# Kernel optimization log

Measured on AMD Instinct MI355X. Metric: run time of the kernel, lower is better.

## Reference

```python
import jax, jax.numpy as jnp
import numpy as np

H = 12          # n_heads
TYPE = 0        # center node type (query path)
EDGES = (0, 4, 5)  # useful_edge for type==0
NEG = -1e10
LN_EPS = 1e-5


def _type_emb(x, W, b, t):
    # Linear(E -> 2E), view [N,2,E], scatter-mask select type t (uniform type -> index)
    h = x @ W.T + b
    N = x.shape[0]
    E = W.shape[0] // 2
    return h.reshape(N, 2, E)[:, t, :]


def _layernorm(x, g, b):
    mu = jnp.mean(x, axis=-1, keepdims=True)
    var = jnp.mean((x - mu) ** 2, axis=-1, keepdims=True)
    return g * (x - mu) / jnp.sqrt(var + LN_EPS) + b


def setup_inputs() -> dict:
    B, L, E, R = 64, 64, 768, 8
    dk = E // H
    key = jax.random.key(0)
    ks = jax.random.split(key, 16)
    s = 0.02
    inp = {
        'center_ids': jax.random.randint(ks[0], (B, L), 0, 5000),
        'centers': jax.random.normal(ks[1], (B * L, E), jnp.float32),
        'all_embs': jax.random.normal(ks[2], (2 * B * L, E), jnp.float32),
        'pre_mask': (jax.random.uniform(ks[3], (B, L, L)) < 0.3).astype(jnp.float32),
        'back_mask': (jax.random.uniform(ks[4], (B, L, L)) < 0.3).astype(jnp.float32),
        'click_mask': (jax.random.uniform(ks[5], (B, L, L)) < 0.3).astype(jnp.float32),
        'blank': jnp.zeros((B, L, L), jnp.float32),
        'Wq': jax.random.normal(ks[6], (2 * E, E), jnp.float32) * s,
        'bq': jnp.zeros((2 * E,), jnp.float32),
        'Wk': jax.random.normal(ks[7], (2 * E, E), jnp.float32) * s,
        'bk': jnp.zeros((2 * E,), jnp.float32),
        'Wv': jax.random.normal(ks[8], (2 * E, E), jnp.float32) * s,
        'bv': jnp.zeros((2 * E,), jnp.float32),
        'Wa': jax.random.normal(ks[9], (2 * E, E), jnp.float32) * s,
        'ba': jnp.zeros((2 * E,), jnp.float32),
        'relation_pri': jnp.ones((R, H), jnp.float32),
        'relation_att': jax.random.normal(ks[10], (R, H, dk, dk), jnp.float32) / np.sqrt(dk),
        'relation_msg': jax.random.normal(ks[11], (R, H, dk, dk), jnp.float32) / np.sqrt(dk),
        'skip': jnp.ones((3,), jnp.float32),
        'ln_gamma': jnp.ones((E,), jnp.float32),
        'ln_beta': jnp.zeros((E,), jnp.float32),
    }
    return inp


def reference(center_ids, centers, all_embs, pre_mask, back_mask, click_mask, blank,
              Wq, bq, Wk, bk, Wv, bv, Wa, ba,
              relation_pri, relation_att, relation_msg, skip, ln_gamma, ln_beta):
    B, L = center_ids.shape
    E = centers.shape[-1]
    dk = E // H
    BL = B * L
    sqrt_dk = np.sqrt(dk).astype(np.float32)

    # type-masked QKV projections (q: all type 0; k,v: first BL type 0, second BL type 1)
    q = _type_emb(centers, Wq, bq, TYPE)                       # [BL, E]
    hk = (all_embs @ Wk.T + bk).reshape(2 * BL, 2, E)
    k = jnp.concatenate([hk[:BL, 0], hk[BL:, 1]], axis=0)      # [2BL, E]
    hv = (all_embs @ Wv.T + bv).reshape(2 * BL, 2, E)
    v = jnp.concatenate([hv[:BL, 0], hv[BL:, 1]], axis=0)      # [2BL, E]

    q4 = q.reshape(B, L, H, dk).transpose(2, 0, 1, 3)                          # [H,B,L,dk]
    k4 = k.reshape(2, B, L, H, dk).transpose(3, 1, 0, 2, 4).reshape(H, B, 2 * L, dk)
    v4 = v.reshape(2, B, L, H, dk).transpose(3, 1, 0, 2, 4).reshape(H, B, 2 * L, dk)

    eidx = jnp.array(EDGES)
    ra = relation_att[eidx]   # [3,H,dk,dk]
    rm = relation_msg[eidx]   # [3,H,dk,dk]
    pri = relation_pri[eidx]  # [3,H]

    kproj = jnp.einsum('hbtd,ehdf->ehbtf', k4, ra)                                  # [3,H,B,2L,dk]
    att = jnp.einsum('hbld,ehbtd->ehblt', q4, kproj) * pri[:, :, None, None, None] / sqrt_dk
    msg = jnp.einsum('hbtd,ehdf->ehbtf', v4, rm)                                    # [3,H,B,2L,dk]

    # flatten (kv_pos, edge) in the torch cat/view order: index = t*3 + e
    A = att.transpose(1, 2, 3, 4, 0).reshape(H, B, L, 2 * L * 3)
    msgf = msg.transpose(1, 2, 3, 0, 4).reshape(H, B, 2 * L * 3, dk)

    # per-edge masks for type==0: edge0 -> [blank|click], edge1 -> [back|blank], edge2 -> [pre|blank]
    m0 = jnp.concatenate([blank, click_mask], axis=-1)
    m1 = jnp.concatenate([back_mask, blank], axis=-1)
    m2 = jnp.concatenate([pre_mask, blank], axis=-1)
    mask = jnp.stack([m0, m1, m2], axis=-1).reshape(B, L, 2 * L * 3) > 0            # [B,L,TE]

    # share masks among identical center ids (equality is transitive => one matmul = closure)
    same = center_ids[:, :, None] == center_ids[:, None, :]                         # [B,L,L]
    repeat = jnp.triu(same, 1).sum(1) > 0                                           # [B,L]
    add = jnp.einsum('bil,blj->bij', same.astype(jnp.float32), mask.astype(jnp.float32)) > 0
    mask = (mask | add) & (~repeat[:, :, None])

    scores = jnp.where(mask[None], A, NEG)
    p = jax.nn.softmax(scores, axis=-1) * mask[None].astype(A.dtype)
    neigh = jnp.einsum('hblt,hbtd->hbld', p, msgf).transpose(1, 2, 0, 3).reshape(BL, E)
    neigh = jax.nn.gelu(neigh, approximate=False)

    retype = _type_emb(neigh, Wa, ba, TYPE)
    alpha = jax.nn.sigmoid(skip[TYPE])
    res = retype * alpha + centers * (1.0 - alpha)
    out = _layernorm(res, ln_gamma, ln_beta)
    return out.reshape(B, L, E)
```

## Files before the change

kernel.cpp:

```cpp
#include <hip/hip_runtime.h>
#include <cmath>

#define NEGV -1e10f

typedef __bf16 bf16_t;
typedef bf16_t bf16x8 __attribute__((ext_vector_type(8)));
typedef bf16_t bf16x4 __attribute__((ext_vector_type(4)));
typedef float f32x4 __attribute__((ext_vector_type(4)));

typedef const __attribute__((address_space(1))) void* gas1p;
typedef __attribute__((address_space(3))) void* las3p;

#define MFMA __builtin_amdgcn_mfma_f32_16x16x32_bf16

__global__ __launch_bounds__(256)
void prep_kernel(const int* __restrict__ ids, const float* __restrict__ pre,
                 const float* __restrict__ back, const float* __restrict__ click,
                 unsigned long long* __restrict__ msk64,
                 const float* __restrict__ rmsg, const float* __restrict__ ratt,
                 const float* __restrict__ pri, bf16_t* __restrict__ rmT, bf16_t* __restrict__ raB,
                 const float* __restrict__ s0, bf16_t* __restrict__ d0,
                 const float* __restrict__ s1, bf16_t* __restrict__ d1,
                 const float* __restrict__ s2, bf16_t* __restrict__ d2,
                 const float* __restrict__ s3, bf16_t* __restrict__ d3,
                 const float* __restrict__ s4, bf16_t* __restrict__ d4,
                 const float* __restrict__ s5, bf16_t* __restrict__ d5) {
  const int bid = blockIdx.x, tid = threadIdx.x;
  __shared__ float pm[64][68], bmm[64][68], cm[64][68];
  __shared__ unsigned long long sbits[64];
  __shared__ unsigned long long colbits[384];
  __shared__ int sid[64];
  __shared__ unsigned char srep[64];
  if (bid < 64) {
    const int b = bid;
    for (int r = 0; r < 4; ++r) {
      int idx = r*256 + tid; int row = idx >> 4; int c4 = (idx & 15) * 4;
      *(float4*)&pm[row][c4]  = *(const float4*)(pre   + (size_t)b*4096 + row*64 + c4);
      *(float4*)&bmm[row][c4] = *(const float4*)(back  + (size_t)b*4096 + row*64 + c4);
      *(float4*)&cm[row][c4]  = *(const float4*)(click + (size_t)b*4096 + row*64 + c4);
    }
    if (tid < 64) sid[tid] = ids[b*64 + tid];
    __syncthreads();
    if (tid < 64) {
      int myid = sid[tid];
      unsigned long long bits = 0ull; int rep = 0;
      for (int l = 0; l < 64; ++l) {
        bool eq = (sid[l] == myid);
        bits |= ((unsigned long long)eq) << l;
        rep |= (eq && (l < tid)) ? 1 : 0;
      }
      sbits[tid] = bits; srep[tid] = (unsigned char)rep;
    }
    for (int j = tid; j < 384; j += 256) {
      int e = j >> 7, t = j & 127;
      unsigned long long cb = 0ull;
      if (e == 0) {
        if (t >= 64) { int tt = t - 64; for (int l = 0; l < 64; ++l) cb |= ((unsigned long long)(cm[l][tt] > 0.0f)) << l; }
      } else if (e == 1) {
        if (t < 64) { for (int l = 0; l < 64; ++l) cb |= ((unsigned long long)(bmm[l][t] > 0.0f)) << l; }
      } else {
        if (t < 64) { for (int l = 0; l < 64; ++l) cb |= ((unsigned long long)(pm[l][t] > 0.0f)) << l; }
      }
      colbits[j] = cb;
    }
    __syncthreads();
    for (int idx = tid; idx < 384; idx += 256) {
      int l = idx / 6, w = idx - l*6;
      unsigned long long r = 0ull;
      if (!srep[l]) {
        unsigned long long sb = sbits[l];
        const int base = w*64;
        for (int jj = 0; jj < 64; ++jj)
          r |= (unsigned long long)((sb & colbits[base + jj]) != 0ull) << jj;
      }
      msk64[((size_t)(b*64) + l)*6 + w] = r;
    }
    return;
  }
  if (bid < 100) {
    const int eh = bid - 64;
    const int e = eh / 12, h = eh - e*12;
    const int re = (e==0) ? 0 : (e==1 ? 4 : 5);
    const float scale = pri[re*12 + h] * 0.125f;
    for (int i = 0; i < 16; ++i) {
      int idx = i*256 + tid;
      int d = idx >> 6, f = idx & 63;
      rmT[((size_t)(e*12 + h)*64 + d)*64 + f] =
          (bf16_t)rmsg[((size_t)(re*12 + h)*64 + f)*64 + d];
      raB[((size_t)(e*12 + h)*64 + d)*64 + f] =
          (bf16_t)(ratt[((size_t)(re*12 + h)*64 + d)*64 + f] * scale);
    }
    return;
  }
  const int N0=786432, N1=1572864, N2=147456, N3=294912, N4=294912, N5=147456;
  const int T = N0+N1+N2+N3+N4+N5;
  int i = (bid - 100) * 256 + tid;
  const int stride = (gridDim.x - 100) * 256;
  for (; i < T; i += stride) {
    const float* s; bf16_t* d; int j = i;
    if (j < N0) { s = s0; d = d0; }
    else { j -= N0; if (j < N1) { s = s1; d = d1; }
    else { j -= N1; if (j < N2) { s = s2; d = d2; }
    else { j -= N2; if (j < N3) { s = s3; d = d3; }
    else { j -= N3; if (j < N4) { s = s4; d = d4; }
    else { j -= N4; s = s5; d = d5; } } } } }
    float4 v = *(const float4*)(s + (size_t)j * 4);
    bf16x4 o = { (bf16_t)v.x, (bf16_t)v.y, (bf16_t)v.z, (bf16_t)v.w };
    *(bf16x4*)(d + (size_t)j * 4) = o;
  }
}

__global__ __launch_bounds__(256)
void proj_mfmaB(const bf16_t* __restrict__ X, const bf16_t* __restrict__ W,
                const float* __restrict__ bias, bf16_t* __restrict__ Y) {
  __shared__ bf16_t As[128 * 32];
  __shared__ bf16_t Bs[128 * 32];
  const int bn = blockIdx.x, bm = blockIdx.y;
  const int row0 = bm * 128, col0 = bn * 128;
  const int tid = threadIdx.x, wave = tid >> 6, lane = tid & 63;
  const int wr = wave >> 1, wc = wave & 1;
  f32x4 acc[4][4] = {};
  const int arow = wr * 64 + (lane & 15);
  const int bcol = wc * 64 + (lane & 15);
  const int koff = (lane >> 4) * 8;
  for (int k0 = 0; k0 < 768; k0 += 32) {
    __syncthreads();
    #pragma unroll
    for (int i = 0; i < 2; ++i) {
      int c = i * 256 + tid; int r = c >> 2; int c8 = (c & 3) * 8;
      __builtin_amdgcn_global_load_lds((gas1p)(X + (size_t)(row0 + r) * 768 + k0 + c8),
                                       (las3p)(As + c * 8), 16, 0, 0);
      __builtin_amdgcn_global_load_lds((gas1p)(W + (size_t)(col0 + r) * 768 + k0 + c8),
                                       (las3p)(Bs + c * 8), 16, 0, 0);
    }
    __syncthreads();
    bf16x8 af[4], bfr[4];
    #pragma unroll
    for (int m = 0; m < 4; ++m) af[m]  = *(const bf16x8*)(As + (arow + m * 16) * 32 + koff);
    #pragma unroll
    for (int n = 0; n < 4; ++n) bfr[n] = *(const bf16x8*)(Bs + (bcol + n * 16) * 32 + koff);
    #pragma unroll
    for (int m = 0; m < 4; ++m)
      #pragma unroll
      for (int n = 0; n < 4; ++n)
        acc[m][n] = MFMA(af[m], bfr[n], acc[m][n], 0, 0, 0);
  }
  const int ocol0 = col0 + wc * 64 + (lane & 15);
  const int orow0 = row0 + wr * 64 + (lane >> 4) * 4;
  #pragma unroll
  for (int n = 0; n < 4; ++n) {
    const int col = ocol0 + n * 16;
    const float bvl = bias[col];
    #pragma unroll
    for (int m = 0; m < 4; ++m)
      #pragma unroll
      for (int r = 0; r < 4; ++r)
        Y[(size_t)(orow0 + m * 16 + r) * 768 + col] = (bf16_t)(acc[m][n][r] + bvl);
  }
}

__global__ __launch_bounds__(256)
void proj_mfmaF(const bf16_t* __restrict__ X, const bf16_t* __restrict__ W,
                const float* __restrict__ bias, float* __restrict__ Y) {
  __shared__ bf16_t As[128 * 32];
  __shared__ bf16_t Bs[128 * 32];
  const int bn = blockIdx.x, bm = blockIdx.y;
  const int row0 = bm * 128, col0 = bn * 128;
  const int tid = threadIdx.x, wave = tid >> 6, lane = tid & 63;
  const int wr = wave >> 1, wc = wave & 1;
  f32x4 acc[4][4] = {};
  const int arow = wr * 64 + (lane & 15);
  const int bcol = wc * 64 + (lane & 15);
  const int koff = (lane >> 4) * 8;
  for (int k0 = 0; k0 < 768; k0 += 32) {
    __syncthreads();
    #pragma unroll
    for (int i = 0; i < 2; ++i) {
      int c = i * 256 + tid; int r = c >> 2; int c8 = (c & 3) * 8;
      __builtin_amdgcn_global_load_lds((gas1p)(X + (size_t)(row0 + r) * 768 + k0 + c8),
                                       (las3p)(As + c * 8), 16, 0, 0);
      __builtin_amdgcn_global_load_lds((gas1p)(W + (size_t)(col0 + r) * 768 + k0 + c8),
                                       (las3p)(Bs + c * 8), 16, 0, 0);
    }
    __syncthreads();
    bf16x8 af[4], bfr[4];
    #pragma unroll
    for (int m = 0; m < 4; ++m) af[m]  = *(const bf16x8*)(As + (arow + m * 16) * 32 + koff);
    #pragma unroll
    for (int n = 0; n < 4; ++n) bfr[n] = *(const bf16x8*)(Bs + (bcol + n * 16) * 32 + koff);
    #pragma unroll
    for (int m = 0; m < 4; ++m)
      #pragma unroll
      for (int n = 0; n < 4; ++n)
        acc[m][n] = MFMA(af[m], bfr[n], acc[m][n], 0, 0, 0);
  }
  const int ocol0 = col0 + wc * 64 + (lane & 15);
  const int orow0 = row0 + wr * 64 + (lane >> 4) * 4;
  #pragma unroll
  for (int n = 0; n < 4; ++n) {
    const int col = ocol0 + n * 16;
    const float bvl = bias[col];
    #pragma unroll
    for (int m = 0; m < 4; ++m)
      #pragma unroll
      for (int r = 0; r < 4; ++r)
        Y[(size_t)(orow0 + m * 16 + r) * 768 + col] = acc[m][n][r] + bvl;
  }
}

__global__ __launch_bounds__(256)
void kv_proj(const bf16_t* __restrict__ X, const bf16_t* __restrict__ Wk,
             const bf16_t* __restrict__ Wv, const float* __restrict__ bk,
             const float* __restrict__ bv, bf16_t* __restrict__ K, bf16_t* __restrict__ VT) {
  __shared__ bf16_t As[128 * 32];
  __shared__ bf16_t Bks[128 * 32];
  __shared__ bf16_t Bvs[128 * 32];
  __shared__ char tl[128 * 256];
  const int bn = blockIdx.x, bm = blockIdx.y;
  const int s = (bm >= 32) ? 1 : 0;
  const int row0 = bm * 128, col0 = bn * 128;
  const int tid = threadIdx.x, wave = tid >> 6, lane = tid & 63;
  const int wr = wave >> 1, wc = wave & 1;
  f32x4 acck[4][4] = {};
  f32x4 accv[4][4] = {};
  const int arow = wr * 64 + (lane & 15);
  const int bcol = wc * 64 + (lane & 15);
  const int koff = (lane >> 4) * 8;
  const bf16_t* Wkb = Wk + (size_t)s * 768 * 768;
  const bf16_t* Wvb = Wv + (size_t)s * 768 * 768;
  for (int k0 = 0; k0 < 768; k0 += 32) {
    __syncthreads();
    #pragma unroll
    for (int i = 0; i < 2; ++i) {
      int c = i * 256 + tid; int r = c >> 2; int c8 = (c & 3) * 8;
      __builtin_amdgcn_global_load_lds((gas1p)(X   + (size_t)(row0 + r) * 768 + k0 + c8),
                                       (las3p)(As  + c * 8), 16, 0, 0);
      __builtin_amdgcn_global_load_lds((gas1p)(Wkb + (size_t)(col0 + r) * 768 + k0 + c8),
                                       (las3p)(Bks + c * 8), 16, 0, 0);
      __builtin_amdgcn_global_load_lds((gas1p)(Wvb + (size_t)(col0 + r) * 768 + k0 + c8),
                                       (las3p)(Bvs + c * 8), 16, 0, 0);
    }
    __syncthreads();
    bf16x8 af[4], bk_[4], bv_[4];
    #pragma unroll
    for (int m = 0; m < 4; ++m) af[m]  = *(const bf16x8*)(As  + (arow + m * 16) * 32 + koff);
    #pragma unroll
    for (int n = 0; n < 4; ++n) { bk_[n] = *(const bf16x8*)(Bks + (bcol + n * 16) * 32 + koff);
                                  bv_[n] = *(const bf16x8*)(Bvs + (bcol + n * 16) * 32 + koff); }
    #pragma unroll
    for (int m = 0; m < 4; ++m)
      #pragma unroll
      for (int n = 0; n < 4; ++n) {
        acck[m][n] = MFMA(af[m], bk_[n], acck[m][n], 0, 0, 0);
        accv[m][n] = MFMA(af[m], bv_[n], accv[m][n], 0, 0, 0);
      }
  }
  const int ocol0 = col0 + wc * 64 + (lane & 15);
  const int orow0 = row0 + wr * 64 + (lane >> 4) * 4;
  #pragma unroll
  for (int n = 0; n < 4; ++n) {
    const int col = ocol0 + n * 16;
    const float bvl = bk[s * 768 + col];
    #pragma unroll
    for (int m = 0; m < 4; ++m)
      #pragma unroll
      for (int r = 0; r < 4; ++r)
        K[(size_t)(orow0 + m * 16 + r) * 768 + col] = (bf16_t)(acck[m][n][r] + bvl);
  }
  #pragma unroll
  for (int n = 0; n < 4; ++n) {
    const int cl = wc * 64 + n * 16 + (lane & 15);
    const float bvl = bv[s * 768 + col0 + cl];
    #pragma unroll
    for (int m = 0; m < 4; ++m)
      #pragma unroll
      for (int r = 0; r < 4; ++r) {
        const int rl = wr * 64 + m * 16 + (lane >> 4) * 4 + r;
        *(bf16_t*)(tl + ((cl * 256 + rl * 2) ^ ((cl & 7) << 4))) = (bf16_t)(accv[m][n][r] + bvl);
      }
  }
  __syncthreads();
  for (int i = 0; i < 8; ++i) {
    int idx = i * 256 + tid; int c = idx >> 4; int t0 = (idx & 15) * 8;
    bf16x8 v = *(const bf16x8*)(tl + ((c * 256 + t0 * 2) ^ ((c & 7) << 4)));
    *(bf16x8*)(VT + (size_t)(col0 + c) * 8192 + row0 + t0) = v;
  }
}

__global__ __launch_bounds__(256, 2)
void attn_fused2(const bf16_t* __restrict__ qraw, const bf16_t* __restrict__ kb,
                 const bf16_t* __restrict__ vT, const bf16_t* __restrict__ rmT,
                 const bf16_t* __restrict__ raB,
                 const unsigned long long* __restrict__ msk64,
                 bf16_t* __restrict__ neigh) {
  const int h = blockIdx.x, b = blockIdx.y;
  __shared__ char lds[81920];
  char* const QLS  = lds;
  char* const RALS = lds + 8192;
  char* const QELS = lds + 32768;
  char* const VLS  = lds;
  char* const PLS  = lds + 16384;
  char* const KLS  = lds + 32768;
  char* const RMLS = lds + 49152;
  char* const USS  = lds + 73728;
  const int tid = threadIdx.x, wave = tid >> 6, lane = tid & 63;
  const int band = wave * 16, colb = lane & 15;

  bf16x8 qreg[2], rareg[6], kreg[4], vreg[4], rmreg[6];
  #pragma unroll
  for (int i = 0; i < 2; ++i) { int idx = i*256 + tid; int l = idx >> 3, f0 = (idx & 7) * 8;
    qreg[i] = *(const bf16x8*)(qraw + (size_t)(b*64 + l)*768 + h*64 + f0); }
  #pragma unroll
  for (int i = 0; i < 6; ++i) { int idx = i*256 + tid; int e = idx >> 9, rem = idx & 511, d = rem >> 3, f0 = (rem & 7) * 8;
    rareg[i] = *(const bf16x8*)(raB + (size_t)((e*12 + h)*64 + d)*64 + f0); }
  #pragma unroll
  for (int i = 0; i < 4; ++i) { int idx = i*256 + tid; int t = idx >> 3, c8 = (idx & 7) * 8;
    int srow = (t >> 6)*4096 + b*64 + (t & 63);
    kreg[i] = *(const bf16x8*)(kb + (size_t)srow*768 + h*64 + c8); }
  #pragma unroll
  for (int i = 0; i < 4; ++i) { int idx = i*256 + tid; int f = idx >> 4, t0 = (idx & 15) * 8;
    vreg[i] = *(const bf16x8*)(vT + (size_t)(h*64 + f)*8192 + (t0 >> 6)*4096 + b*64 + (t0 & 63)); }
  #pragma unroll
  for (int i = 0; i < 6; ++i) { int idx = i*256 + tid; int e = idx >> 9, rem = idx & 511, d = rem >> 3, f0 = (rem & 7) * 8;
    rmreg[i] = *(const bf16x8*)(rmT + (size_t)((e*12 + h)*64 + d)*64 + f0); }

  #pragma unroll
  for (int i = 0; i < 2; ++i) { int idx = i*256 + tid; int l = idx >> 3, f0 = (idx & 7) * 8;
    *(bf16x8*)(QLS + ((l*128 + f0*2) ^ ((l & 7) << 4))) = qreg[i]; }
  #pragma unroll
  for (int i = 0; i < 6; ++i) { int idx = i*256 + tid; int e = idx >> 9, rem = idx & 511, d = rem >> 3, f0 = (rem & 7) * 8;
    *(bf16x8*)(RALS + e*8192 + ((d*128 + f0*2) ^ ((d & 7) << 4))) = rareg[i]; }
  __syncthreads();
  f32x4 accq[3][4] = {};
  #pragma unroll
  for (int ks = 0; ks < 2; ++ks) {
    const int kb2 = (ks*32 + (lane >> 4)*8) * 2;
    const int la = band + colb;
    bf16x8 a = *(const bf16x8*)(QLS + ((la*128 + kb2) ^ ((la & 7) << 4)));
    #pragma unroll
    for (int e = 0; e < 3; ++e)
      #pragma unroll
      for (int n = 0; n < 4; ++n) {
        int d = n*16 + colb;
        bf16x8 bf = *(const bf16x8*)(RALS + e*8192 + ((d*128 + kb2) ^ ((d & 7) << 4)));
        accq[e][n] = MFMA(a, bf, accq[e][n], 0, 0, 0);
      }
  }
  #pragma unroll
  for (int e = 0; e < 3; ++e)
    #pragma unroll
    for (int n = 0; n < 4; ++n)
      #pragma unroll
      for (int r = 0; r < 4; ++r) {
        int l = band + (lane >> 4)*4 + r, d = n*16 + colb;
        *(bf16_t*)(QELS + e*8192 + ((l*128 + d*2) ^ ((l & 7) << 4))) = (bf16_t)accq[e][n][r];
      }
  __syncthreads();
  bf16x8 af[3][2];
  #pragma unroll
  for (int e = 0; e < 3; ++e)
    #pragma unroll
    for (int ks = 0; ks < 2; ++ks) {
      int la = band + colb, kd2 = (ks*32 + (lane >> 4)*8) * 2;
      af[e][ks] = *(const bf16x8*)(QELS + e*8192 + ((la*128 + kd2) ^ ((la & 7) << 4)));
    }
  __syncthreads();
  #pragma unroll
  for (int i = 0; i < 4; ++i) { int idx = i*256 + tid; int t = idx >> 3, c8 = (idx & 7) * 8;
    *(bf16x8*)(KLS + ((t*128 + c8*2) ^ ((t & 7) << 4))) = kreg[i]; }
  #pragma unroll
  for (int i = 0; i < 4; ++i) { int idx = i*256 + tid; int f = idx >> 4, t0 = (idx & 15) * 8;
    *(bf16x8*)(VLS + ((f*256 + t0*2) ^ ((f & 7) << 4))) = vreg[i]; }
  #pragma unroll
  for (int i = 0; i < 6; ++i) { int idx = i*256 + tid; int e = idx >> 9, rem = idx & 511, d = rem >> 3, f0 = (rem & 7) * 8;
    *(bf16x8*)(RMLS + e*8192 + ((d*128 + f0*2) ^ ((d & 7) << 4))) = rmreg[i]; }
  __syncthreads();
  f32x4 acc[3][8] = {};
  #pragma unroll
  for (int ks = 0; ks < 2; ++ks) {
    bf16x8 bfr[8];
    #pragma unroll
    for (int n = 0; n < 8; ++n) {
      int t = n*16 + colb;
      bfr[n] = *(const bf16x8*)(KLS + ((t*128 + (ks*32 + (lane >> 4)*8)*2) ^ ((t & 7) << 4)));
    }
    #pragma unroll
    for (int e = 0; e < 3; ++e)
      #pragma unroll
      for (int n = 0; n < 8; ++n)
        acc[e][n] = MFMA(af[e][ks], bfr[n], acc[e][n], 0, 0, 0);
  }
  float mx[4], inv[4];
  #pragma unroll
  for (int r = 0; r < 4; ++r) {
    const int l = band + (lane >> 4)*4 + r;
    const unsigned long long* mr = msk64 + (size_t)(b*64 + l)*6;
    #pragma unroll
    for (int e = 0; e < 3; ++e) {
      unsigned long long w0 = mr[e*2], w1 = mr[e*2 + 1];
      #pragma unroll
      for (int n = 0; n < 8; ++n) {
        unsigned long long w = (n < 4) ? w0 : w1;
        int bitpos = (n*16 + colb) & 63;
        if (!((w >> bitpos) & 1ull)) acc[e][n][r] = NEGV;
      }
    }
  }
  #pragma unroll
  for (int r = 0; r < 4; ++r) {
    float m = NEGV;
    #pragma unroll
    for (int e = 0; e < 3; ++e)
      #pragma unroll
      for (int n = 0; n < 8; ++n) m = fmaxf(m, acc[e][n][r]);
    #pragma unroll
    for (int off = 1; off < 16; off <<= 1) m = fmaxf(m, __shfl_xor(m, off, 64));
    mx[r] = m;
  }
  #pragma unroll
  for (int r = 0; r < 4; ++r) {
    float s = 0.0f;
    #pragma unroll
    for (int e = 0; e < 3; ++e)
      #pragma unroll
      for (int n = 0; n < 8; ++n) {
        float v = __expf(acc[e][n][r] - mx[r]);
        acc[e][n][r] = v; s += v;
      }
    #pragma unroll
    for (int off = 1; off < 16; off <<= 1) s += __shfl_xor(s, off, 64);
    inv[r] = (mx[r] < -5e9f) ? 0.0f : 1.0f / s;
  }
  f32x4 accN[4] = {};
  #pragma unroll
  for (int e = 0; e < 3; ++e) {
    #pragma unroll
    for (int n = 0; n < 8; ++n)
      #pragma unroll
      for (int r = 0; r < 4; ++r) {
        int l = band + (lane >> 4)*4 + r;
        int t = n*16 + colb;
        *(bf16_t*)(PLS + ((l*256 + t*2) ^ ((l & 7) << 4))) = (bf16_t)(acc[e][n][r] * inv[r]);
      }
    __syncthreads();
    f32x4 accU[4] = {};
    #pragma unroll
    for (int ks = 0; ks < 4; ++ks) {
      const int kb2 = (ks*32 + (lane >> 4)*8) * 2;
      const int la = band + colb;
      bf16x8 a = *(const bf16x8*)(PLS + ((la*256 + kb2) ^ ((la & 7) << 4)));
      #pragma unroll
      for (int n = 0; n < 4; ++n) {
        int f = n*16 + colb;
        bf16x8 bv = *(const bf16x8*)(VLS + ((f*256 + kb2) ^ ((f & 7) << 4)));
        accU[n] = MFMA(a, bv, accU[n], 0, 0, 0);
      }
    }
    #pragma unroll
    for (int n = 0; n < 4; ++n)
      #pragma unroll
      for (int r = 0; r < 4; ++r) {
        int l = band + (lane >> 4)*4 + r;
        int f = n*16 + colb;
        *(bf16_t*)(USS + ((l*128 + f*2) ^ ((l & 7) << 4))) = (bf16_t)accU[n][r];
      }
    __syncthreads();
    #pragma unroll
    for (int ks = 0; ks < 2; ++ks) {
      const int kb2 = (ks*32 + (lane >> 4)*8) * 2;
      const int la = band + colb;
      bf16x8 a2 = *(const bf16x8*)(USS + ((la*128 + kb2) ^ ((la & 7) << 4)));
      #pragma unroll
      for (int n = 0; n < 4; ++n) {
        int d = n*16 + colb;
        bf16x8 brm = *(const bf16x8*)(RMLS + e*8192 + ((d*128 + kb2) ^ ((d & 7) << 4)));
        accN[n] = MFMA(a2, brm, accN[n], 0, 0, 0);
      }
    }
  }
  #pragma unroll
  for (int n = 0; n < 4; ++n)
    #pragma unroll
    for (int r = 0; r < 4; ++r) {
      int l = band + (lane >> 4)*4 + r;
      int d = n*16 + colb;
      float x = accN[n][r];
      float g = 0.5f * x * (1.0f + erff(x * 0.70710678118654752f));
      neigh[(size_t)(b*64 + l)*768 + h*64 + d] = (bf16_t)g;
    }
}

__global__ __launch_bounds__(256)
void ln_kernel(const float* __restrict__ rt, const float* __restrict__ centers,
               const float* __restrict__ skip, const float* __restrict__ gamma,
               const float* __restrict__ beta, float* __restrict__ out) {
  const int row  = blockIdx.x*4 + (threadIdx.x >> 6);
  const int lane = threadIdx.x & 63;
  const float alpha = 1.0f / (1.0f + expf(-skip[0]));
  const float* rp = rt + (size_t)row*768;
  const float* cp = centers + (size_t)row*768;
  float r[12];
  float sum = 0.0f;
  #pragma unroll
  for (int c = 0; c < 12; ++c) {
    int j = lane + 64*c;
    float x = alpha*rp[j] + (1.0f - alpha)*cp[j];
    r[c] = x; sum += x;
  }
  #pragma unroll
  for (int off = 1; off < 64; off <<= 1) sum += __shfl_xor(sum, off, 64);
  float mean = sum * (1.0f/768.0f);
  float vsum = 0.0f;
  #pragma unroll
  for (int c = 0; c < 12; ++c) { float d = r[c] - mean; vsum += d*d; }
  #pragma unroll
  for (int off = 1; off < 64; off <<= 1) vsum += __shfl_xor(vsum, off, 64);
  float inv = 1.0f / sqrtf(vsum * (1.0f/768.0f) + 1e-5f);
  #pragma unroll
  for (int c = 0; c < 12; ++c) {
    int j = lane + 64*c;
    out[(size_t)row*768 + j] = gamma[j]*(r[c] - mean)*inv + beta[j];
  }
}

extern "C" void kernel_launch(void* const* d_in, const int* in_sizes, int n_in,
                              void* d_out, int out_size, void* d_ws, size_t ws_size,
                              hipStream_t stream) {
  const int*   ids     = (const int*)  d_in[0];
  const float* centers = (const float*)d_in[1];
  const float* allemb  = (const float*)d_in[2];
  const float* pre     = (const float*)d_in[3];
  const float* back    = (const float*)d_in[4];
  const float* click   = (const float*)d_in[5];
  const float* Wq = (const float*)d_in[7];
  const float* bq = (const float*)d_in[8];
  const float* Wk = (const float*)d_in[9];
  const float* bk = (const float*)d_in[10];
  const float* Wv = (const float*)d_in[11];
  const float* bv = (const float*)d_in[12];
  const float* Wa = (const float*)d_in[13];
  const float* ba = (const float*)d_in[14];
  const float* pri  = (const float*)d_in[15];
  const float* ratt = (const float*)d_in[16];
  const float* rmsg = (const float*)d_in[17];
  const float* skip = (const float*)d_in[18];
  const float* gam  = (const float*)d_in[19];
  const float* bet  = (const float*)d_in[20];
  float* out = (float*)d_out;

  char* wp = (char*)d_ws;
  bf16_t* cen_bf = (bf16_t*)wp;  wp += 6291456;
  bf16_t* all_bf = (bf16_t*)wp;  wp += 12582912;
  bf16_t* Wq_bf  = (bf16_t*)wp;  wp += 1179648;
  bf16_t* Wk_bf  = (bf16_t*)wp;  wp += 2359296;
  bf16_t* Wv_bf  = (bf16_t*)wp;  wp += 2359296;
  bf16_t* Wa_bf  = (bf16_t*)wp;  wp += 1179648;
  bf16_t* rmT    = (bf16_t*)wp;  wp += 294912;
  bf16_t* raB    = (bf16_t*)wp;  wp += 294912;
  bf16_t* qraw   = (bf16_t*)wp;  wp += 6291456;
  bf16_t* kb     = (bf16_t*)wp;  wp += 12582912;
  bf16_t* vTb    = (bf16_t*)wp;  wp += 12582912;
  unsigned long long* msk64 = (unsigned long long*)wp; wp += 196608;
  bf16_t* neighb = (bf16_t*)wp;  wp += 6291456;
  float*  rt     = (float*)wp;   wp += 12582912;

  prep_kernel<<<dim3(2048), 256, 0, stream>>>(
      ids, pre, back, click, msk64, rmsg, ratt, pri, rmT, raB,
      centers, cen_bf, allemb, all_bf, Wq, Wq_bf, Wk, Wk_bf, Wv, Wv_bf, Wa, Wa_bf);

  proj_mfmaB<<<dim3(6, 32), 256, 0, stream>>>(cen_bf, Wq_bf, bq, qraw);
  kv_proj   <<<dim3(6, 64), 256, 0, stream>>>(all_bf, Wk_bf, Wv_bf, bk, bv, kb, vTb);

  attn_fused2<<<dim3(12, 64), 256, 0, stream>>>(qraw, kb, vTb, rmT, raB, msk64, neighb);

  proj_mfmaF<<<dim3(6, 32), 256, 0, stream>>>(neighb, Wa_bf, ba, rt);
  ln_kernel<<<dim3(1024), 256, 0, stream>>>(rt, centers, skip, gam, bet, out);
}
```

Measured before the change: 266.8 us.

## Merge Q and KV projections into one double-buffered launch

Replaces the separate Q projection and KV projection kernels with a single qkv_proj kernel whose grid covers both: the first 32 row-blocks do the Q GEMM and the rest do the fused K/V GEMM. The k-loop now double-buffers its LDS tiles, issuing the next tile's async global-to-LDS loads before computing on the current one, with one barrier per step instead of two. This removes one kernel launch and tail, lets Q and KV blocks share the GPU together, and overlaps load latency with MFMA work. The cost is more LDS per block (48KB), which may lower occupancy, plus a Q/KV branch that mixes light and heavy blocks in one grid.

```diff
diff --git a/kernel.cpp b/kernel.cpp
--- a/kernel.cpp
+++ b/kernel.cpp
@@ -111,51 +111,137 @@
 }
 
 __global__ __launch_bounds__(256)
-void proj_mfmaB(const bf16_t* __restrict__ X, const bf16_t* __restrict__ W,
-                const float* __restrict__ bias, bf16_t* __restrict__ Y) {
-  __shared__ bf16_t As[128 * 32];
-  __shared__ bf16_t Bs[128 * 32];
-  const int bn = blockIdx.x, bm = blockIdx.y;
+void qkv_proj(const bf16_t* __restrict__ cen, const bf16_t* __restrict__ allb,
+              const bf16_t* __restrict__ Wq, const bf16_t* __restrict__ Wk,
+              const bf16_t* __restrict__ Wv,
+              const float* __restrict__ bq, const float* __restrict__ bk,
+              const float* __restrict__ bv,
+              bf16_t* __restrict__ Q, bf16_t* __restrict__ K, bf16_t* __restrict__ VT) {
+  __shared__ char lds[49152];
+  const int bn = blockIdx.x, by = blockIdx.y;
+  const bool qmode = (by < 32);
+  const int bm = qmode ? by : (by - 32);
+  const int s = (!qmode && bm >= 32) ? 1 : 0;
   const int row0 = bm * 128, col0 = bn * 128;
+  const bf16_t* X  = qmode ? cen : allb;
+  const bf16_t* WA = qmode ? Wq : (Wk + (size_t)s * 768 * 768);
+  const bf16_t* WB = Wv + (size_t)s * 768 * 768;
   const int tid = threadIdx.x, wave = tid >> 6, lane = tid & 63;
   const int wr = wave >> 1, wc = wave & 1;
-  f32x4 acc[4][4] = {};
   const int arow = wr * 64 + (lane & 15);
   const int bcol = wc * 64 + (lane & 15);
   const int koff = (lane >> 4) * 8;
-  for (int k0 = 0; k0 < 768; k0 += 32) {
-    __syncthreads();
+  f32x4 acck[4][4] = {};
+  f32x4 accv[4][4] = {};
+
+  {
+    bf16_t* As  = (bf16_t*)(lds);
+    bf16_t* Bks = As + 4096;
+    bf16_t* Bvs = As + 8192;
     #pragma unroll
     for (int i = 0; i < 2; ++i) {
       int c = i * 256 + tid; int r = c >> 2; int c8 = (c & 3) * 8;
-      __builtin_amdgcn_global_load_lds((gas1p)(X + (size_t)(row0 + r) * 768 + k0 + c8),
+      __builtin_amdgcn_global_load_lds((gas1p)(X  + (size_t)(row0 + r) * 768 + c8),
                                        (las3p)(As + c * 8), 16, 0, 0);
-      __builtin_amdgcn_global_load_lds((gas1p)(W + (size_t)(col0 + r) * 768 + k0 + c8),
-                                       (las3p)(Bs + c * 8), 16, 0, 0);
-    }
-    __syncthreads();
-    bf16x8 af[4], bfr[4];
-    #pragma unroll
-    for (int m = 0; m < 4; ++m) af[m]  = *(const bf16x8*)(As + (arow + m * 16) * 32 + koff);
-    #pragma unroll
-    for (int n = 0; n < 4; ++n) bfr[n] = *(const bf16x8*)(Bs + (bcol + n * 16) * 32 + koff);
-    #pragma unroll
-    for (int m = 0; m < 4; ++m)
-      #pragma unroll
-      for (int n = 0; n < 4; ++n)
-        acc[m][n] = MFMA(af[m], bfr[n], acc[m][n], 0, 0, 0);
-  }
+      __builtin_amdgcn_global_load_lds((gas1p)(WA + (size_t)(col0 + r) * 768 + c8),
+                                       (las3p)(Bks + c * 8), 16, 0, 0);
+      if (!qmode)
+        __builtin_amdgcn_global_load_lds((gas1p)(WB + (size_t)(col0 + r) * 768 + c8),
+                                         (las3p)(Bvs + c * 8), 16, 0, 0);
+    }
+  }
+  __syncthreads();
+
+  for (int k = 0; k < 24; ++k) {
+    if (k < 23) {
+      const int k0 = (k + 1) * 32;
+      bf16_t* As  = (bf16_t*)(lds + ((k + 1) & 1) * 24576);
+      bf16_t* Bks = As + 4096;
+      bf16_t* Bvs = As + 8192;
+      #pragma unroll
+      for (int i = 0; i < 2; ++i) {
+        int c = i * 256 + tid; int r = c >> 2; int c8 = (c & 3) * 8;
+        __builtin_amdgcn_global_load_lds((gas1p)(X  + (size_t)(row0 + r) * 768 + k0 + c8),
+                                         (las3p)(As + c * 8), 16, 0, 0);
+        __builtin_amdgcn_global_load_lds((gas1p)(WA + (size_t)(col0 + r) * 768 + k0 + c8),
+                                         (las3p)(Bks + c * 8), 16, 0, 0);
+        if (!qmode)
+          __builtin_amdgcn_global_load_lds((gas1p)(WB + (size_t)(col0 + r) * 768 + k0 + c8),
+                                           (las3p)(Bvs + c * 8), 16, 0, 0);
+      }
+    }
+    {
+      bf16_t* As  = (bf16_t*)(lds + (k & 1) * 24576);
+      bf16_t* Bks = As + 4096;
+      bf16_t* Bvs = As + 8192;
+      bf16x8 af[4], bk_[4], bv_[4];
+      #pragma unroll
+      for (int m = 0; m < 4; ++m) af[m]  = *(const bf16x8*)(As  + (arow + m * 16) * 32 + koff);
+      #pragma unroll
+      for (int n = 0; n < 4; ++n) bk_[n] = *(const bf16x8*)(Bks + (bcol + n * 16) * 32 + koff);
+      if (!qmode) {
+        #pragma unroll
+        for (int n = 0; n < 4; ++n) bv_[n] = *(const bf16x8*)(Bvs + (bcol + n * 16) * 32 + koff);
+      }
+      #pragma unroll
+      for (int m = 0; m < 4; ++m)
+        #pragma unroll
+        for (int n = 0; n < 4; ++n)
+          acck[m][n] = MFMA(af[m], bk_[n], acck[m][n], 0, 0, 0);
+      if (!qmode) {
+        #pragma unroll
+        for (int m = 0; m < 4; ++m)
+          #pragma unroll
+          for (int n = 0; n < 4; ++n)
+            accv[m][n] = MFMA(af[m], bv_[n], accv[m][n], 0, 0, 0);
+      }
+    }
+    __syncthreads();
+  }
+
   const int ocol0 = col0 + wc * 64 + (lane & 15);
   const int orow0 = row0 + wr * 64 + (lane >> 4) * 4;
+  if (qmode) {
+    #pragma unroll
+    for (int n = 0; n < 4; ++n) {
+      const int col = ocol0 + n * 16;
+      const float bvl = bq[col];
+      #pragma unroll
+      for (int m = 0; m < 4; ++m)
+        #pragma unroll
+        for (int r = 0; r < 4; ++r)
+          Q[(size_t)(orow0 + m * 16 + r) * 768 + col] = (bf16_t)(acck[m][n][r] + bvl);
+    }
+    return;
+  }
   #pragma unroll
   for (int n = 0; n < 4; ++n) {
     const int col = ocol0 + n * 16;
-    const float bvl = bias[col];
+    const float bvl = bk[s * 768 + col];
     #pragma unroll
     for (int m = 0; m < 4; ++m)
       #pragma unroll
       for (int r = 0; r < 4; ++r)
-        Y[(size_t)(orow0 + m * 16 + r) * 768 + col] = (bf16_t)(acc[m][n][r] + bvl);
+        K[(size_t)(orow0 + m * 16 + r) * 768 + col] = (bf16_t)(acck[m][n][r] + bvl);
+  }
+  char* const tl = lds + 16384;
+  #pragma unroll
+  for (int n = 0; n < 4; ++n) {
+    const int cl = wc * 64 + n * 16 + (lane & 15);
+    const float bvl = bv[s * 768 + col0 + cl];
+    #pragma unroll
+    for (int m = 0; m < 4; ++m)
+      #pragma unroll
+      for (int r = 0; r < 4; ++r) {
+        const int rl = wr * 64 + m * 16 + (lane >> 4) * 4 + r;
+        *(bf16_t*)(tl + ((cl * 256 + rl * 2) ^ ((cl & 7) << 4))) = (bf16_t)(accv[m][n][r] + bvl);
+      }
+  }
+  __syncthreads();
+  for (int i = 0; i < 8; ++i) {
+    int idx = i * 256 + tid; int c = idx >> 4; int t0 = (idx & 15) * 8;
+    bf16x8 v = *(const bf16x8*)(tl + ((c * 256 + t0 * 2) ^ ((c & 7) << 4)));
+    *(bf16x8*)(VT + (size_t)(col0 + c) * 8192 + row0 + t0) = v;
   }
 }
 
@@ -205,85 +291,6 @@
       #pragma unroll
       for (int r = 0; r < 4; ++r)
         Y[(size_t)(orow0 + m * 16 + r) * 768 + col] = acc[m][n][r] + bvl;
-  }
-}
-
-__global__ __launch_bounds__(256)
-void kv_proj(const bf16_t* __restrict__ X, const bf16_t* __restrict__ Wk,
-             const bf16_t* __restrict__ Wv, const float* __restrict__ bk,
-             const float* __restrict__ bv, bf16_t* __restrict__ K, bf16_t* __restrict__ VT) {
-  __shared__ bf16_t As[128 * 32];
-  __shared__ bf16_t Bks[128 * 32];
-  __shared__ bf16_t Bvs[128 * 32];
-  __shared__ char tl[128 * 256];
-  const int bn = blockIdx.x, bm = blockIdx.y;
-  const int s = (bm >= 32) ? 1 : 0;
-  const int row0 = bm * 128, col0 = bn * 128;
-  const int tid = threadIdx.x, wave = tid >> 6, lane = tid & 63;
-  const int wr = wave >> 1, wc = wave & 1;
-  f32x4 acck[4][4] = {};
-  f32x4 accv[4][4] = {};
-  const int arow = wr * 64 + (lane & 15);
-  const int bcol = wc * 64 + (lane & 15);
-  const int koff = (lane >> 4) * 8;
-  const bf16_t* Wkb = Wk + (size_t)s * 768 * 768;
-  const bf16_t* Wvb = Wv + (size_t)s * 768 * 768;
-  for (int k0 = 0; k0 < 768; k0 += 32) {
-    __syncthreads();
-    #pragma unroll
-    for (int i = 0; i < 2; ++i) {
-      int c = i * 256 + tid; int r = c >> 2; int c8 = (c & 3) * 8;
-      __builtin_amdgcn_global_load_lds((gas1p)(X   + (size_t)(row0 + r) * 768 + k0 + c8),
-                                       (las3p)(As  + c * 8), 16, 0, 0);
-      __builtin_amdgcn_global_load_lds((gas1p)(Wkb + (size_t)(col0 + r) * 768 + k0 + c8),
-                                       (las3p)(Bks + c * 8), 16, 0, 0);
-      __builtin_amdgcn_global_load_lds((gas1p)(Wvb + (size_t)(col0 + r) * 768 + k0 + c8),
-                                       (las3p)(Bvs + c * 8), 16, 0, 0);
-    }
-    __syncthreads();
-    bf16x8 af[4], bk_[4], bv_[4];
-    #pragma unroll
-    for (int m = 0; m < 4; ++m) af[m]  = *(const bf16x8*)(As  + (arow + m * 16) * 32 + koff);
-    #pragma unroll
-    for (int n = 0; n < 4; ++n) { bk_[n] = *(const bf16x8*)(Bks + (bcol + n * 16) * 32 + koff);
-                                  bv_[n] = *(const bf16x8*)(Bvs + (bcol + n * 16) * 32 + koff); }
-    #pragma unroll
-    for (int m = 0; m < 4; ++m)
-      #pragma unroll
-      for (int n = 0; n < 4; ++n) {
-        acck[m][n] = MFMA(af[m], bk_[n], acck[m][n], 0, 0, 0);
-        accv[m][n] = MFMA(af[m], bv_[n], accv[m][n], 0, 0, 0);
-      }
-  }
-  const int ocol0 = col0 + wc * 64 + (lane & 15);
-  const int orow0 = row0 + wr * 64 + (lane >> 4) * 4;
-  #pragma unroll
-  for (int n = 0; n < 4; ++n) {
-    const int col = ocol0 + n * 16;
-    const float bvl = bk[s * 768 + col];
-    #pragma unroll
-    for (int m = 0; m < 4; ++m)
-      #pragma unroll
-      for (int r = 0; r < 4; ++r)
-        K[(size_t)(orow0 + m * 16 + r) * 768 + col] = (bf16_t)(acck[m][n][r] + bvl);
-  }
-  #pragma unroll
-  for (int n = 0; n < 4; ++n) {
-    const int cl = wc * 64 + n * 16 + (lane & 15);
-    const float bvl = bv[s * 768 + col0 + cl];
-    #pragma unroll
-    for (int m = 0; m < 4; ++m)
-      #pragma unroll
-      for (int r = 0; r < 4; ++r) {
-        const int rl = wr * 64 + m * 16 + (lane >> 4) * 4 + r;
-        *(bf16_t*)(tl + ((cl * 256 + rl * 2) ^ ((cl & 7) << 4))) = (bf16_t)(accv[m][n][r] + bvl);
-      }
-  }
-  __syncthreads();
-  for (int i = 0; i < 8; ++i) {
-    int idx = i * 256 + tid; int c = idx >> 4; int t0 = (idx & 15) * 8;
-    bf16x8 v = *(const bf16x8*)(tl + ((c * 256 + t0 * 2) ^ ((c & 7) << 4)));
-    *(bf16x8*)(VT + (size_t)(col0 + c) * 8192 + row0 + t0) = v;
   }
 }
 
@@ -568,8 +575,8 @@
       ids, pre, back, click, msk64, rmsg, ratt, pri, rmT, raB,
       centers, cen_bf, allemb, all_bf, Wq, Wq_bf, Wk, Wk_bf, Wv, Wv_bf, Wa, Wa_bf);
 
-  proj_mfmaB<<<dim3(6, 32), 256, 0, stream>>>(cen_bf, Wq_bf, bq, qraw);
-  kv_proj   <<<dim3(6, 64), 256, 0, stream>>>(all_bf, Wk_bf, Wv_bf, bk, bv, kb, vTb);
+  qkv_proj<<<dim3(6, 96), 256, 0, stream>>>(cen_bf, all_bf, Wq_bf, Wk_bf, Wv_bf,
+                                            bq, bk, bv, qraw, kb, vTb);
 
   attn_fused2<<<dim3(12, 64), 256, 0, stream>>>(qraw, kb, vTb, rmT, raB, msk64, neighb);
 
```

After: 248.9 us. 1.07x faster.
